# Kernel optimization log

Measured on AMD Instinct MI355X. Metric: run time of the kernel, lower is better.

The kernel has to match this reference:

```python
import jax, jax.numpy as jnp
import numpy as np

B, S, NODE, DEP, R, L, E = 32, 1024, 256, 64, 50, 16, 128


def setup_inputs() -> dict:
    key = jax.random.key(0)
    k1, k2, k3, k4, k5 = jax.random.split(key, 5)
    context = jax.random.normal(k1, (B, S, NODE), dtype=jnp.float32)
    # torch.rand -> uniform [0,1); one [dep, node+dep] matrix per dependency relation
    dep_W = jax.random.uniform(k2, (R, DEP, NODE + DEP), dtype=jnp.float32)
    heads = jax.random.randint(k3, (B, L, E), 0, S, dtype=jnp.int32)
    tails = jax.random.randint(k4, (B, L, E), 0, S, dtype=jnp.int32)
    rels = jax.random.randint(k5, (B, L, E), 0, R, dtype=jnp.int32)
    return {"context": context, "dep_W": dep_W, "heads": heads, "tails": tails, "rels": rels}


def reference(context, dep_W, heads, tails, rels):
    # context: [B,S,node]; dep_W: [R,dep,node+dep]; heads/tails/rels: [B,L,E]
    B_, S_, node = context.shape
    dep = dep_W.shape[1]
    E_ = heads.shape[2]
    batch_off = jnp.arange(B_, dtype=jnp.int32)[:, None] * S_  # [B,1]

    def layer_step(child, layer):
        h, t, r = layer  # each [B,E]
        # gather per-edge tail features (node feature ++ child state from deeper layers)
        ctx_t = jnp.take_along_axis(context, t[:, :, None], axis=1)  # [B,E,node]
        chd_t = jnp.take_along_axis(child, t[:, :, None], axis=1)    # [B,E,dep]
        feat = jnp.concatenate([ctx_t, chd_t], axis=-1)              # [B,E,node+dep]
        W_e = dep_W[r]                                               # [B,E,dep,node+dep]
        # sum(W * feat, dim=1) == relation-indexed matvec
        msg = jnp.einsum('bekd,bed->bek', W_e, feat)                 # [B,E,dep]
        # scatter-average messages onto head nodes (per batch -> flat index)
        idx = (batch_off + h).reshape(-1)                            # [B*E]
        seg = jax.ops.segment_sum(msg.reshape(-1, dep), idx, num_segments=B_ * S_)
        cnt = jax.ops.segment_sum(jnp.ones((B_ * E_,), msg.dtype), idx, num_segments=B_ * S_)
        avg = seg / jnp.maximum(cnt, 1.0)[:, None]
        child_flat = child.reshape(B_ * S_, dep)
        # heads touched this layer get the averaged message (assignment semantics)
        child_new = jnp.where((cnt > 0)[:, None], avg, child_flat).reshape(B_, S_, dep)
        return child_new, None

    child0 = jnp.zeros((B_, S_, dep), context.dtype)
    layers = (jnp.moveaxis(heads, 1, 0), jnp.moveaxis(tails, 1, 0), jnp.moveaxis(rels, 1, 0))
    child, _ = jax.lax.scan(layer_step, child0, layers)  # layer 0 = deepest layer
    return jnp.concatenate([context, child], axis=-1)    # [B,S,node+dep]
```

## Files before the change

### kernel.cpp

```cpp
#include <hip/hip_runtime.h>

constexpr int B_ = 32;
constexpr int S_ = 1024;
constexpr int NODE_ = 256;
constexpr int DEP_ = 64;
constexpr int R_ = 50;
constexpr int L_ = 16;
constexpr int E_ = 128;
constexpr int FEAT_ = NODE_ + DEP_;
constexpr int NEDGE_ = B_ * E_;
constexpr int BS_ = B_ * S_;
constexpr int CH_ = 16;
constexpr int NCH_ = 320;
constexpr int PREB_ = 512;
constexpr int GCH_ = 64;
constexpr int NGC_ = 1088;

constexpr size_t N_CHILD  = (size_t)BS_ * DEP_;
constexpr size_t OFF_A0   = N_CHILD;
constexpr size_t OFF_WT   = N_CHILD * 4;
constexpr size_t N_WT     = (size_t)R_ * FEAT_ * DEP_;
constexpr size_t OFF_SORT = OFF_WT + N_WT;
constexpr size_t N_SORT   = (size_t)L_ * NEDGE_;
constexpr size_t OFF_CHUNK= OFF_SORT + N_SORT;
constexpr size_t N_CHUNK_I= (size_t)L_ * NCH_ * 4;
constexpr size_t OFF_HC   = OFF_CHUNK + N_CHUNK_I;
constexpr size_t N_HC     = (size_t)L_ * BS_;
constexpr size_t OFF_MT   = OFF_HC + N_HC;
constexpr size_t OFF_MH   = OFF_MT + N_SORT;
constexpr size_t OFF_MI   = OFF_MH + N_SORT;
constexpr size_t OFF_CD   = OFF_MI + N_SORT;
constexpr size_t N_CD     = (size_t)L_ * NEDGE_ * DEP_;
constexpr size_t OFF_GIDX = OFF_CD + N_CD;
constexpr size_t OFF_GCH  = OFF_GIDX + N_SORT;

__global__ void k_pre(const float* __restrict__ W, const int* __restrict__ rels,
                      const int* __restrict__ heads,
                      float* __restrict__ WT2, int* __restrict__ sorted,
                      int4* __restrict__ chunks, int* __restrict__ hc,
                      float* __restrict__ zero_base) {
  int blk = blockIdx.x, tid = threadIdx.x;
  if (blk < L_) {
    int l = blk;
    __shared__ int hist[R_], startA[R_], rank[R_], cstart[R_];
    __shared__ int ntot;
    if (tid < R_) { hist[tid] = 0; rank[tid] = 0; }
    int* hcl = hc + (size_t)l * BS_;
    for (int i = tid; i < BS_; i += 256) hcl[i] = 0;
    __syncthreads();
    for (int ed = tid; ed < NEDGE_; ed += 256) {
      int b = ed >> 7, e = ed & (E_ - 1);
      atomicAdd(&hist[rels[(b * L_ + l) * E_ + e]], 1);
      atomicAdd(&hcl[b * S_ + heads[(b * L_ + l) * E_ + e]], 1);
    }
    __syncthreads();
    if (tid == 0) {
      int s = 0, cs = 0;
      for (int r = 0; r < R_; ++r) {
        startA[r] = s; s += hist[r];
        cstart[r] = cs; cs += (hist[r] + CH_ - 1) / CH_;
      }
      ntot = cs;
    }
    __syncthreads();
    for (int ed = tid; ed < NEDGE_; ed += 256) {
      int b = ed >> 7, e = ed & (E_ - 1);
      int r = rels[(b * L_ + l) * E_ + e];
      int pos = startA[r] + atomicAdd(&rank[r], 1);
      sorted[l * NEDGE_ + pos] = ed;
    }
    if (tid < R_) {
      int n = hist[tid], st = startA[tid], cs = cstart[tid];
      for (int m = 0; m * CH_ < n; ++m) {
        int c = n - m * CH_; if (c > CH_) c = CH_;
        chunks[l * NCH_ + cs + m] = make_int4(tid, st + m * CH_, c, 0);
      }
    }
    __syncthreads();
    for (int i = ntot + tid; i < NCH_; i += 256)
      chunks[l * NCH_ + i] = make_int4(0, 0, 0, 0);
  } else {
    int gtid = (blk - L_) * 256 + tid;
    const int NT = PREB_ * 256;
    for (int gid = gtid; gid < (int)N_WT; gid += NT) {
      int r = gid / 20480;
      int rem = gid - r * 20480;
      int i4 = rem >> 8;
      int k = (rem >> 2) & 63;
      int c = rem & 3;
      WT2[gid] = W[((size_t)r * DEP_ + k) * FEAT_ + 4 * i4 + c];
    }
    float4* z4 = (float4*)zero_base;
    int nz4 = (int)((N_CHILD * 2) / 4);
    for (int i = gtid; i < nz4; i += NT) z4[i] = make_float4(0.f, 0.f, 0.f, 0.f);
  }
}

__global__ void k_gbin(const int4* __restrict__ chunks, int* __restrict__ gidx,
                       int4* __restrict__ gchunks) {
  __shared__ int ghist[R_], goff[R_], grank[R_], gcs[R_];
  int tid = threadIdx.x;
  if (tid < R_) { ghist[tid] = 0; grank[tid] = 0; }
  __syncthreads();
  for (int i = tid; i < L_ * NCH_; i += 1024) {
    int4 ck = chunks[i];
    if (ck.z > 0) atomicAdd(&ghist[ck.x], ck.z);
  }
  __syncthreads();
  if (tid == 0) {
    int s = 0, cs = 0;
    for (int r = 0; r < R_; ++r) {
      goff[r] = s; s += ghist[r];
      gcs[r] = cs; cs += (ghist[r] + GCH_ - 1) / GCH_;
    }
  }
  __syncthreads();
  for (int i = tid; i < L_ * NCH_; i += 1024) {
    int4 ck = chunks[i];
    if (ck.z > 0) {
      int l = i / NCH_;
      int base = atomicAdd(&grank[ck.x], ck.z);
      for (int m = 0; m < ck.z; ++m)
        gidx[goff[ck.x] + base + m] = l * NEDGE_ + ck.y + m;
    }
  }
  __syncthreads();
  if (tid < R_) {
    int n = ghist[tid], go = goff[tid], cs = gcs[tid];
    for (int m = 0; m * GCH_ < n; ++m) {
      int c = n - m * GCH_; if (c > GCH_) c = GCH_;
      gchunks[cs + m] = make_int4(tid, go + m * GCH_, c, 0);
    }
  }
  __syncthreads();
  int ntot = gcs[R_ - 1] + (ghist[R_ - 1] + GCH_ - 1) / GCH_;
  for (int i = ntot + tid; i < NGC_; i += 1024)
    gchunks[i] = make_int4(0, 0, 0, 0);
}

__device__ __forceinline__ float dot64(const float4* __restrict__ f4,
                                       const float4* __restrict__ w) {
  float a0 = 0.f, a1 = 0.f, a2 = 0.f, a3 = 0.f;
#pragma unroll
  for (int i = 0; i < 16; ++i) {
    float4 f = f4[i];
    a0 = fmaf(w[i].x, f.x, a0);
    a1 = fmaf(w[i].y, f.y, a1);
    a2 = fmaf(w[i].z, f.z, a2);
    a3 = fmaf(w[i].w, f.w, a3);
  }
  return (a0 + a1) + (a2 + a3);
}

__device__ __forceinline__ void fma4(float& a, float4 w, float4 f) {
  a = fmaf(w.x, f.x, a);
  a = fmaf(w.y, f.y, a);
  a = fmaf(w.z, f.z, a);
  a = fmaf(w.w, f.w, a);
}

__global__ void __launch_bounds__(256, 4) k_ctx2(
    const float* __restrict__ context, const float* __restrict__ WT2,
    const int* __restrict__ heads, const int* __restrict__ tails,
    const int* __restrict__ sorted, const int4* __restrict__ gchunks,
    const int* __restrict__ gidx, const int* __restrict__ hc,
    float* __restrict__ ctxdot, int* __restrict__ m_trow,
    int* __restrict__ m_hrow, float* __restrict__ m_invc) {
  int4 ck = gchunks[blockIdx.x];
  int r = ck.x, gstart = ck.y, gcnt = ck.z;
  if (gcnt == 0) return;
  int tid = threadIdx.x;
  int tk = tid & 15, tj = tid >> 4;

  __shared__ float4 Wn_s[16 * 64];
  __shared__ __align__(16) float F_s[GCH_][68];
  __shared__ int   trow_s[GCH_];
  __shared__ float invc_s[GCH_];
  __shared__ int   pos_s[GCH_];

  if (tid < GCH_) {
    int jj = (tid < gcnt) ? tid : (gcnt - 1);
    int pos = gidx[gstart + jj];
    int l = pos >> 12;
    int ed = sorted[pos];
    int b = ed >> 7, e = ed & (E_ - 1);
    int t = tails[(b * L_ + l) * E_ + e];
    int h = heads[(b * L_ + l) * E_ + e];
    int trow = b * S_ + t, hrow = b * S_ + h;
    float invc = 1.0f / (float)hc[(size_t)l * BS_ + hrow];
    trow_s[tid] = trow;
    invc_s[tid] = invc;
    pos_s[tid] = pos;
    if (tid < gcnt) {
      int tch = (l > 0) && (hc[(size_t)(l - 1) * BS_ + trow] > 0);
      m_trow[pos] = trow | (tch ? (int)0x80000000 : 0);
      m_hrow[pos] = hrow;
      m_invc[pos] = invc;
    }
  }
  __syncthreads();

  float acc[4][4] = {};
  const float4* ctx4 = (const float4*)context;
  const float4* W4 = (const float4*)WT2 + (size_t)r * 80 * 64;

  int jrow = tid >> 2;
  int c0 = tid & 3;
  int trowj = trow_s[jrow];

  for (int dp = 0; dp < 4; ++dp) {
#pragma unroll
    for (int rep = 0; rep < 4; ++rep) {
      int idx = tid + 256 * rep;
      Wn_s[idx] = W4[1024 * dp + idx];
    }
#pragma unroll
    for (int rep = 0; rep < 4; ++rep) {
      int c4 = c0 + 4 * rep;
      float4 v = ctx4[(size_t)trowj * 64 + dp * 16 + c4];
      *(float4*)&F_s[jrow][4 * c4] = v;
    }
    __syncthreads();

#pragma unroll
    for (int i4 = 0; i4 < 16; ++i4) {
      float4 wv[4], fv[4];
#pragma unroll
      for (int a = 0; a < 4; ++a) wv[a] = Wn_s[i4 * 64 + 4 * tk + a];
#pragma unroll
      for (int bb = 0; bb < 4; ++bb)
        fv[bb] = *(const float4*)&F_s[4 * tj + bb][4 * i4];
#pragma unroll
      for (int a = 0; a < 4; ++a)
#pragma unroll
        for (int bb = 0; bb < 4; ++bb) fma4(acc[a][bb], wv[a], fv[bb]);
    }
    __syncthreads();
  }

#pragma unroll
  for (int bb = 0; bb < 4; ++bb) {
    int j = 4 * tj + bb;
    if (j < gcnt) {
      float iv = invc_s[j];
      float4 o;
      o.x = acc[0][bb] * iv;
      o.y = acc[1][bb] * iv;
      o.z = acc[2][bb] * iv;
      o.w = acc[3][bb] * iv;
      ((float4*)ctxdot)[(size_t)pos_s[j] * 16 + tk] = o;
    }
  }
}

__global__ void __launch_bounds__(256) k_layer(
    const float* __restrict__ WT2, float* __restrict__ child,
    const int4* __restrict__ chunks, const int* __restrict__ m_trow,
    const int* __restrict__ m_hrow, const float* __restrict__ m_invc,
    const float* __restrict__ ctxdot, int l,
    const float* __restrict__ Aprev, float* __restrict__ Acur,
    float* __restrict__ Anext) {
  int tid = threadIdx.x;
  int4 ck = chunks[l * NCH_ + blockIdx.x];
  int r = ck.x, start = ck.y, ccnt = ck.z;
  __shared__ float feat[CH_][DEP_];

  if (ccnt > 0) {
    int wv = tid >> 6, k = tid & 63;

    const float4* Wp = (const float4*)WT2 + ((size_t)r * 80 + 64) * 64 + k;
    float4 w[16];
#pragma unroll
    for (int i = 0; i < 16; ++i) w[i] = Wp[(size_t)i * 64];

    int jj[4], valid[4], tch[4], trow[4], hrow[4];
    float invc[4];
#pragma unroll
    for (int u = 0; u < 4; ++u) {
      int j = wv + 4 * u;
      valid[u] = (j < ccnt);
      jj[u] = valid[u] ? j : (ccnt - 1);
      int pos = l * NEDGE_ + start + jj[u];
      int tr = m_trow[pos];
      tch[u] = (tr < 0);
      trow[u] = tr & 0x7fffffff;
      hrow[u] = m_hrow[pos];
      invc[u] = m_invc[pos];
    }

    float v[4];
#pragma unroll
    for (int u = 0; u < 4; ++u) {
      const float* p = tch[u] ? Aprev : child;
      v[u] = p[(size_t)trow[u] * DEP_ + k];
    }
#pragma unroll
    for (int u = 0; u < 4; ++u) feat[jj[u]][k] = v[u];
    __syncthreads();

#pragma unroll
    for (int u = 0; u < 4; ++u) {
      float d = dot64((const float4*)&feat[jj[u]][0], w);
      int pos = l * NEDGE_ + start + jj[u];
      float contrib = d * invc[u] + ctxdot[(size_t)pos * DEP_ + k];
      if (valid[u]) atomicAdd(&Acur[(size_t)hrow[u] * DEP_ + k], contrib);
    }
  }

  int gtid = blockIdx.x * 256 + tid;
  const int NT = NCH_ * 256;
  if (l > 0) {
    const float4* Ap4 = (const float4*)Aprev;
    float4* ch4 = (float4*)child;
    const int* mh = m_hrow + (size_t)(l - 1) * NEDGE_;
    for (int idx = gtid; idx < NEDGE_ * 16; idx += NT) {
      int pos = idx >> 4, c4 = idx & 15;
      int hrow = mh[pos];
      ch4[(size_t)hrow * 16 + c4] = Ap4[(size_t)hrow * 16 + c4];
    }
  }
  if (l + 1 < L_) {
    float4* An4 = (float4*)Anext;
    const int* mh = m_hrow + (size_t)(l + 1) * NEDGE_;
    float4 z = make_float4(0.f, 0.f, 0.f, 0.f);
    for (int idx = gtid; idx < NEDGE_ * 16; idx += NT) {
      int pos = idx >> 4, c4 = idx & 15;
      An4[(size_t)mh[pos] * 16 + c4] = z;
    }
  }
}

__global__ void k_out(const float4* __restrict__ ctx4,
                      const float4* __restrict__ chd4,
                      const float4* __restrict__ A04,
                      const int* __restrict__ hc15,
                      float4* __restrict__ out4) {
  constexpr int TOT4 = B_ * S_ * (FEAT_ / 4);
  int i = blockIdx.x * blockDim.x + threadIdx.x;
  if (i >= TOT4) return;
  int row = i / 80;
  int c4 = i - row * 80;
  float4 v;
  if (c4 < 64) {
    v = ctx4[(size_t)row * 64 + c4];
  } else {
    int k4 = c4 - 64;
    v = (hc15[row] > 0) ? A04[(size_t)row * 16 + k4]
                        : chd4[(size_t)row * 16 + k4];
  }
  out4[i] = v;
}

extern "C" void kernel_launch(void* const* d_in, const int* in_sizes, int n_in,
                              void* d_out, int out_size, void* d_ws, size_t ws_size,
                              hipStream_t stream) {
  const float* context = (const float*)d_in[0];
  const float* dep_W   = (const float*)d_in[1];
  const int*   heads   = (const int*)d_in[2];
  const int*   tails   = (const int*)d_in[3];
  const int*   rels    = (const int*)d_in[4];
  float* out = (float*)d_out;

  float* ws = (float*)d_ws;
  float* child  = ws;
  float* A[3] = { ws + OFF_A0, ws + OFF_A0 + N_CHILD, ws + OFF_A0 + 2 * N_CHILD };
  float* WT2    = ws + OFF_WT;
  int*   sorted = (int*)(ws + OFF_SORT);
  int4*  chunks = (int4*)(ws + OFF_CHUNK);
  int*   hc     = (int*)(ws + OFF_HC);
  int*   m_trow = (int*)(ws + OFF_MT);
  int*   m_hrow = (int*)(ws + OFF_MH);
  float* m_invc = ws + OFF_MI;
  float* ctxdot = ws + OFF_CD;
  int*   gidx   = (int*)(ws + OFF_GIDX);
  int4*  gchunks= (int4*)(ws + OFF_GCH);

  k_pre<<<L_ + PREB_, 256, 0, stream>>>(dep_W, rels, heads, WT2, sorted,
                                        chunks, hc, child);

  k_gbin<<<1, 1024, 0, stream>>>(chunks, gidx, gchunks);

  k_ctx2<<<NGC_, 256, 0, stream>>>(context, WT2, heads, tails, sorted,
                                   gchunks, gidx, hc, ctxdot, m_trow, m_hrow,
                                   m_invc);

  for (int l = 0; l < L_; ++l) {
    float* Acur  = A[l % 3];
    float* Aprev = A[(l + 2) % 3];
    float* Anext = A[(l + 1) % 3];
    k_layer<<<NCH_, 256, 0, stream>>>(WT2, child, chunks, m_trow, m_hrow,
                                      m_invc, ctxdot, l, Aprev, Acur, Anext);
  }

  constexpr int TOT4 = B_ * S_ * (FEAT_ / 4);
  k_out<<<(TOT4 + 255) / 256, 256, 0, stream>>>(
      (const float4*)context, (const float4*)child, (const float4*)A[0],
      hc + (size_t)(L_ - 1) * BS_, (float4*)out);
}
```

Before: 318.0 us.

## Parallelize global relation binning and prefetch tiles in context matvec

The single-block k_gbin kernel is replaced by k_gidx, which runs one block per (relation, layer) pair. Each block fills its own segment of the global index list using per-layer histograms and offsets that k_pre now saves. Separately, the context-dot kernel double-buffers through registers: it loads the next W and context slice while computing on the current one. It also changes the shared-memory W access to a strided pattern, which alters which output columns each thread owns and makes the output stores scalar. The goal is to remove a serial one-block bottleneck and hide global load latency, at the cost of more registers and uncoalesced scalar stores.

```diff
diff --git a/kernel.cpp b/kernel.cpp
--- a/kernel.cpp
+++ b/kernel.cpp
@@ -33,12 +33,15 @@
 constexpr size_t N_CD     = (size_t)L_ * NEDGE_ * DEP_;
 constexpr size_t OFF_GIDX = OFF_CD + N_CD;
 constexpr size_t OFF_GCH  = OFF_GIDX + N_SORT;
+constexpr size_t OFF_HLR  = OFF_GCH + (size_t)NGC_ * 4;
+constexpr size_t OFF_SLR  = OFF_HLR + (size_t)L_ * R_;
 
 __global__ void k_pre(const float* __restrict__ W, const int* __restrict__ rels,
                       const int* __restrict__ heads,
                       float* __restrict__ WT2, int* __restrict__ sorted,
                       int4* __restrict__ chunks, int* __restrict__ hc,
-                      float* __restrict__ zero_base) {
+                      float* __restrict__ zero_base,
+                      int* __restrict__ hist_lr, int* __restrict__ start_lr) {
   int blk = blockIdx.x, tid = threadIdx.x;
   if (blk < L_) {
     int l = blk;
@@ -70,6 +73,8 @@
       sorted[l * NEDGE_ + pos] = ed;
     }
     if (tid < R_) {
+      hist_lr[l * R_ + tid] = hist[tid];
+      start_lr[l * R_ + tid] = startA[tid];
       int n = hist[tid], st = startA[tid], cs = cstart[tid];
       for (int m = 0; m * CH_ < n; ++m) {
         int c = n - m * CH_; if (c > CH_) c = CH_;
@@ -96,46 +101,58 @@
   }
 }
 
-__global__ void k_gbin(const int4* __restrict__ chunks, int* __restrict__ gidx,
-                       int4* __restrict__ gchunks) {
-  __shared__ int ghist[R_], goff[R_], grank[R_], gcs[R_];
+__global__ void __launch_bounds__(256) k_gidx(
+    const int* __restrict__ hist_lr, const int* __restrict__ start_lr,
+    int* __restrict__ gidx, int4* __restrict__ gchunks) {
+  int bid = blockIdx.x;
+  int r = bid / L_, l = bid - r * L_;
   int tid = threadIdx.x;
-  if (tid < R_) { ghist[tid] = 0; grank[tid] = 0; }
-  __syncthreads();
-  for (int i = tid; i < L_ * NCH_; i += 1024) {
-    int4 ck = chunks[i];
-    if (ck.z > 0) atomicAdd(&ghist[ck.x], ck.z);
-  }
+  __shared__ int sh[L_ * R_];
+  __shared__ int base_s, ntot_s;
+  for (int i = tid; i < L_ * R_; i += 256) sh[i] = hist_lr[i];
   __syncthreads();
   if (tid == 0) {
-    int s = 0, cs = 0;
-    for (int r = 0; r < R_; ++r) {
-      goff[r] = s; s += ghist[r];
-      gcs[r] = cs; cs += (ghist[r] + GCH_ - 1) / GCH_;
-    }
+    int goff = 0;
+    for (int rr = 0; rr < r; ++rr)
+      for (int ll = 0; ll < L_; ++ll) goff += sh[ll * R_ + rr];
+    for (int ll = 0; ll < l; ++ll) goff += sh[ll * R_ + r];
+    base_s = goff;
   }
   __syncthreads();
-  for (int i = tid; i < L_ * NCH_; i += 1024) {
-    int4 ck = chunks[i];
-    if (ck.z > 0) {
-      int l = i / NCH_;
-      int base = atomicAdd(&grank[ck.x], ck.z);
-      for (int m = 0; m < ck.z; ++m)
-        gidx[goff[ck.x] + base + m] = l * NEDGE_ + ck.y + m;
-    }
-  }
-  __syncthreads();
-  if (tid < R_) {
-    int n = ghist[tid], go = goff[tid], cs = gcs[tid];
-    for (int m = 0; m * GCH_ < n; ++m) {
-      int c = n - m * GCH_; if (c > GCH_) c = GCH_;
-      gchunks[cs + m] = make_int4(tid, go + m * GCH_, c, 0);
-    }
-  }
-  __syncthreads();
-  int ntot = gcs[R_ - 1] + (ghist[R_ - 1] + GCH_ - 1) / GCH_;
-  for (int i = ntot + tid; i < NGC_; i += 1024)
-    gchunks[i] = make_int4(0, 0, 0, 0);
+  int n = sh[l * R_ + r];
+  int st = start_lr[l * R_ + r];
+  int base = base_s;
+  for (int i = tid; i < n; i += 256)
+    gidx[base + i] = l * NEDGE_ + st + i;
+
+  if (bid == 0) {
+    __shared__ int tot[R_], goffA[R_], cstart[R_];
+    if (tid < R_) {
+      int t = 0;
+      for (int ll = 0; ll < L_; ++ll) t += sh[ll * R_ + tid];
+      tot[tid] = t;
+    }
+    __syncthreads();
+    if (tid == 0) {
+      int s = 0, cs = 0;
+      for (int rr = 0; rr < R_; ++rr) {
+        goffA[rr] = s; s += tot[rr];
+        cstart[rr] = cs; cs += (tot[rr] + GCH_ - 1) / GCH_;
+      }
+      ntot_s = cs;
+    }
+    __syncthreads();
+    if (tid < R_) {
+      int nn = tot[tid], go = goffA[tid], cs = cstart[tid];
+      for (int m = 0; m * GCH_ < nn; ++m) {
+        int c = nn - m * GCH_; if (c > GCH_) c = GCH_;
+        gchunks[cs + m] = make_int4(tid, go + m * GCH_, c, 0);
+      }
+    }
+    __syncthreads();
+    for (int i = ntot_s + tid; i < NGC_; i += 256)
+      gchunks[i] = make_int4(0, 0, 0, 0);
+  }
 }
 
 __device__ __forceinline__ float dot64(const float4* __restrict__ f4,
@@ -208,25 +225,34 @@
   int c0 = tid & 3;
   int trowj = trow_s[jrow];
 
+  float4 wreg[4], freg[4];
+#pragma unroll
+  for (int rep = 0; rep < 4; ++rep) {
+    wreg[rep] = W4[256 * rep + tid];
+    freg[rep] = ctx4[(size_t)trowj * 64 + (c0 + 4 * rep)];
+  }
+
   for (int dp = 0; dp < 4; ++dp) {
 #pragma unroll
     for (int rep = 0; rep < 4; ++rep) {
-      int idx = tid + 256 * rep;
-      Wn_s[idx] = W4[1024 * dp + idx];
-    }
-#pragma unroll
-    for (int rep = 0; rep < 4; ++rep) {
-      int c4 = c0 + 4 * rep;
-      float4 v = ctx4[(size_t)trowj * 64 + dp * 16 + c4];
-      *(float4*)&F_s[jrow][4 * c4] = v;
-    }
-    __syncthreads();
+      Wn_s[256 * rep + tid] = wreg[rep];
+      *(float4*)&F_s[jrow][4 * (c0 + 4 * rep)] = freg[rep];
+    }
+    __syncthreads();
+
+    if (dp < 3) {
+#pragma unroll
+      for (int rep = 0; rep < 4; ++rep) {
+        wreg[rep] = W4[1024 * (dp + 1) + 256 * rep + tid];
+        freg[rep] = ctx4[(size_t)trowj * 64 + (dp + 1) * 16 + (c0 + 4 * rep)];
+      }
+    }
 
 #pragma unroll
     for (int i4 = 0; i4 < 16; ++i4) {
       float4 wv[4], fv[4];
 #pragma unroll
-      for (int a = 0; a < 4; ++a) wv[a] = Wn_s[i4 * 64 + 4 * tk + a];
+      for (int a = 0; a < 4; ++a) wv[a] = Wn_s[i4 * 64 + tk + 16 * a];
 #pragma unroll
       for (int bb = 0; bb < 4; ++bb)
         fv[bb] = *(const float4*)&F_s[4 * tj + bb][4 * i4];
@@ -243,12 +269,9 @@
     int j = 4 * tj + bb;
     if (j < gcnt) {
       float iv = invc_s[j];
-      float4 o;
-      o.x = acc[0][bb] * iv;
-      o.y = acc[1][bb] * iv;
-      o.z = acc[2][bb] * iv;
-      o.w = acc[3][bb] * iv;
-      ((float4*)ctxdot)[(size_t)pos_s[j] * 16 + tk] = o;
+      float* rowp = ctxdot + (size_t)pos_s[j] * DEP_;
+#pragma unroll
+      for (int a = 0; a < 4; ++a) rowp[tk + 16 * a] = acc[a][bb] * iv;
     }
   }
 }
@@ -374,11 +397,13 @@
   float* ctxdot = ws + OFF_CD;
   int*   gidx   = (int*)(ws + OFF_GIDX);
   int4*  gchunks= (int4*)(ws + OFF_GCH);
+  int*   hist_lr= (int*)(ws + OFF_HLR);
+  int*   start_lr=(int*)(ws + OFF_SLR);
 
   k_pre<<<L_ + PREB_, 256, 0, stream>>>(dep_W, rels, heads, WT2, sorted,
-                                        chunks, hc, child);
-
-  k_gbin<<<1, 1024, 0, stream>>>(chunks, gidx, gchunks);
+                                        chunks, hc, child, hist_lr, start_lr);
+
+  k_gidx<<<R_ * L_, 256, 0, stream>>>(hist_lr, start_lr, gidx, gchunks);
 
   k_ctx2<<<NGC_, 256, 0, stream>>>(context, WT2, heads, tails, sorted,
                                    gchunks, gidx, hc, ctxdot, m_trow, m_hrow,
```

Result: no change. 312.1 us (-1.9%).
